# Performance work log

Measured on AMD Instinct MI355X. Metric: run time of the kernel, lower is better.

Reference implementation:

```python
import jax, jax.numpy as jnp
import numpy as np

PAGE_SIZE = 64  # page size of the 64-token page table (get_page_table_64)


def setup_inputs() -> dict:
    key = jax.random.key(0)
    k1, k2, k3, k4 = jax.random.split(key, 4)
    b, h, d = 64, 64, 128
    num_blocks = 128
    num_pages = b * num_blocks
    query = jax.random.normal(k1, (b, h, d), dtype=jnp.float32)
    weights = jax.random.normal(k2, (b, h), dtype=jnp.float32)
    index_k_cache = jax.random.normal(k3, (num_pages, PAGE_SIZE, d), dtype=jnp.float32)
    # each batch row gets its own distinct pages (all indices in range)
    block_tables = jnp.arange(b * num_blocks, dtype=jnp.int32).reshape(b, num_blocks)
    seq_lens = jax.random.randint(k4, (b,), 1, num_blocks * PAGE_SIZE, dtype=jnp.int32)
    return {
        "query": query,
        "weights": weights,
        "index_k_cache": index_k_cache,
        "block_tables": block_tables,
        "seq_lens": seq_lens,
    }


def reference(query, weights, index_k_cache, block_tables, seq_lens):
    # Faithful translation of triton_mqa_logits_kernel (paged MQA ReLU-weighted
    # QK logits for the top-k indexer).
    b, h, d = query.shape
    num_blocks = block_tables.shape[1]
    max_seq_len = num_blocks * PAGE_SIZE
    # Gather paged KV per block table: [b, num_blocks, PAGE, d] -> [b, S, d]
    k = index_k_cache[block_tables].reshape(b, max_seq_len, d)
    # s[b,h,s] = q . k  (MQA: single K shared across index heads)
    s = jnp.einsum("bhd,bsd->bhs", query, k)
    # ReLU then per-head weighted sum over heads -> [b, S]
    logits = jnp.einsum("bh,bhs->bs", weights, jax.nn.relu(s))
    # positions beyond the sequence length are invalid (-inf, as in the ragged
    # path all_qk_logits init, so downstream top-k never selects them)
    pos = jnp.arange(max_seq_len, dtype=jnp.int32)
    mask = pos[None, :] < seq_lens[:, None]
    return jnp.where(mask, logits, -jnp.inf).astype(jnp.float32)
```

## Files before the change

kernel.cpp:

```cpp
#include <hip/hip_runtime.h>
#include <hip/hip_bf16.h>

#define B 64
#define H 64
#define D 128
#define NB 128
#define PAGE 64
#define SMAX (NB * PAGE)
#define TILE_S 64
#define NEG_BIG (-3.0e38f)

typedef __attribute__((ext_vector_type(8))) short bf16x8;
typedef __attribute__((ext_vector_type(4))) float f32x4;

__device__ __forceinline__ unsigned int rnd16(float f) {
    union { float f; unsigned int u; } v; v.f = f;
    return v.u + 0x8000u;
}
__device__ __forceinline__ unsigned int pack2(float lo, float hi) {
    return __builtin_amdgcn_perm(rnd16(hi), rnd16(lo), 0x07060302);
}
__device__ __forceinline__ bf16x8 cvt8(float4 a, float4 b) {
    union { unsigned int u[4]; bf16x8 v; } r;
    r.u[0] = pack2(a.x, a.y); r.u[1] = pack2(a.z, a.w);
    r.u[2] = pack2(b.x, b.y); r.u[3] = pack2(b.z, b.w);
    return r.v;
}

__device__ __forceinline__ void load_lds16(const void* g, void* l) {
    __builtin_amdgcn_global_load_lds(
        (const __attribute__((address_space(1))) unsigned int*)g,
        (__attribute__((address_space(3))) unsigned int*)l,
        16, 0, 0);
}

__global__ __launch_bounds__(256) void q_prep(
    const float* __restrict__ query, unsigned int* __restrict__ qws)
{
    const int b = blockIdx.x >> 2, i = blockIdx.x & 3, tid = threadIdx.x;
    const float* qb = query + (size_t)b * H * D;
    unsigned int* ob = qws + (size_t)b * 4096;
    const int idx = i * 256 + tid;
    const int h = idx >> 4, c = idx & 15;
    const float4 f0 = *(const float4*)(qb + h * D + c * 8);
    const float4 f1 = *(const float4*)(qb + h * D + c * 8 + 4);
    uint4 o;
    o.x = pack2(f0.x, f0.y); o.y = pack2(f0.z, f0.w);
    o.z = pack2(f1.x, f1.y); o.w = pack2(f1.z, f1.w);
    *(uint4*)(ob + (h * 16 + (c ^ (h & 15))) * 4) = o;
}

__global__ __launch_bounds__(256) void indexer_kernel(
    const unsigned int* __restrict__ qws,
    const float* __restrict__ weights,
    const float* __restrict__ kcache,
    const int*   __restrict__ block_tables,
    const int*   __restrict__ seq_lens,
    float*       __restrict__ out)
{
    const int b    = blockIdx.y;
    const int tile = blockIdx.x;
    const int tid  = threadIdx.x;
    const int slen = seq_lens[b];

    if (tile * TILE_S >= slen) {
        if (tid < TILE_S)
            out[(size_t)b * SMAX + tile * TILE_S + tid] = NEG_BIG;
        return;
    }

    __shared__ __align__(16) float k_lds[TILE_S * D];
    __shared__ __align__(16) unsigned short q_lds[H * 16 * 8];

    const int wv = tid >> 6, ln = tid & 63;
    const int quad = ln >> 4, lm = ln & 15;

    const int page = block_tables[b * NB + tile];
    const float* pbase = kcache + (size_t)page * PAGE * D;

    #pragma unroll
    for (int j = 0; j < 8; ++j) {
        const int r  = wv * 16 + j * 2 + (ln >> 5);
        const int cs = ln & 31;
        const int cg = cs ^ (r & 15);
        load_lds16(pbase + r * D + cg * 4, &k_lds[(wv * 16 + j * 2) * D]);
    }
    {
        const unsigned int* src = qws + (size_t)b * 4096 + wv * 1024;
        #pragma unroll
        for (int j = 0; j < 4; ++j)
            load_lds16(src + j * 256 + ln * 4,
                       &q_lds[(wv * 1024 + j * 256) * 2]);
    }
    __syncthreads();

    const int wbase = tile * TILE_S + wv * 16;
    if (wbase >= slen) {
        if (ln < 16) out[(size_t)b * SMAX + wbase + ln] = NEG_BIG;
        return;
    }

    f32x4 acc[4] = {};
    #pragma unroll
    for (int kc = 0; kc < 4; ++kc) {
        const int row = wv * 16 + lm;
        const int c0  = kc * 8 + quad * 2;
        const float4 f0 = *(const float4*)&k_lds[row * D + ((c0    ) ^ lm) * 4];
        const float4 f1 = *(const float4*)&k_lds[row * D + ((c0 + 1) ^ lm) * 4];
        const bf16x8 a = cvt8(f0, f1);
        #pragma unroll
        for (int ni = 0; ni < 4; ++ni) {
            const int slot = (ni * 16 + lm) * 16 + ((kc * 4 + quad) ^ lm);
            const bf16x8 q = *(const bf16x8*)&q_lds[slot * 8];
            acc[ni] = __builtin_amdgcn_mfma_f32_16x16x32_bf16(a, q, acc[ni], 0, 0, 0);
        }
    }

    float w[4];
    #pragma unroll
    for (int ni = 0; ni < 4; ++ni)
        w[ni] = weights[b * H + ni * 16 + lm];

    #pragma unroll
    for (int r = 0; r < 4; ++r) {
        float v = 0.f;
        #pragma unroll
        for (int ni = 0; ni < 4; ++ni)
            v = fmaf(w[ni], fmaxf(acc[ni][r], 0.f), v);
        v += __shfl_xor(v, 1);
        v += __shfl_xor(v, 2);
        v += __shfl_xor(v, 4);
        v += __shfl_xor(v, 8);
        if (lm == 0) {
            const int pos = wbase + quad * 4 + r;
            out[(size_t)b * SMAX + pos] = (pos < slen) ? v : NEG_BIG;
        }
    }
}

extern "C" void kernel_launch(void* const* d_in, const int* in_sizes, int n_in,
                              void* d_out, int out_size, void* d_ws, size_t ws_size,
                              hipStream_t stream) {
    const float* query   = (const float*)d_in[0];
    const float* weights = (const float*)d_in[1];
    const float* kcache  = (const float*)d_in[2];
    const int*   bt      = (const int*)d_in[3];
    const int*   sl      = (const int*)d_in[4];
    float*       out     = (float*)d_out;
    unsigned int* qws    = (unsigned int*)d_ws;

    q_prep<<<B * 4, 256, 0, stream>>>(query, qws);
    dim3 grid(SMAX / TILE_S, B);
    indexer_kernel<<<grid, 256, 0, stream>>>(qws, weights, kcache, bt, sl, out);
}
```

Before: 333.8 us.

## Drop LDS staging; load K and bf16 Q fragments directly from global memory

Removes the shared-memory staging of the K page and Q tile along with the block-wide barrier, so each lane loads its MFMA operands straight from global memory. The Q preprocessing kernel now writes Q in a fragment-ordered layout so that each lane's per-(kc, ni) bf16x8 load is contiguous. This drops the LDS round-trip and sync and lets waves past the sequence end exit before issuing any loads. In exchange, Q fragments are re-read from global/L2 by every block and K loads become per-lane 32-byte strided accesses rather than asynchronous LDS copies.

```diff
diff --git a/kernel.cpp b/kernel.cpp
--- a/kernel.cpp
+++ b/kernel.cpp
@@ -1,5 +1,4 @@
 #include <hip/hip_runtime.h>
-#include <hip/hip_bf16.h>
 
 #define B 64
 #define H 64
@@ -27,27 +26,19 @@
     return r.v;
 }
 
-__device__ __forceinline__ void load_lds16(const void* g, void* l) {
-    __builtin_amdgcn_global_load_lds(
-        (const __attribute__((address_space(1))) unsigned int*)g,
-        (__attribute__((address_space(3))) unsigned int*)l,
-        16, 0, 0);
-}
-
 __global__ __launch_bounds__(256) void q_prep(
     const float* __restrict__ query, unsigned int* __restrict__ qws)
 {
     const int b = blockIdx.x >> 2, i = blockIdx.x & 3, tid = threadIdx.x;
-    const float* qb = query + (size_t)b * H * D;
-    unsigned int* ob = qws + (size_t)b * 4096;
     const int idx = i * 256 + tid;
-    const int h = idx >> 4, c = idx & 15;
-    const float4 f0 = *(const float4*)(qb + h * D + c * 8);
-    const float4 f1 = *(const float4*)(qb + h * D + c * 8 + 4);
+    const int c = idx >> 6, h = idx & 63;
+    const float* src = query + ((size_t)b * H + h) * D + c * 8;
+    const float4 f0 = *(const float4*)(src);
+    const float4 f1 = *(const float4*)(src + 4);
     uint4 o;
     o.x = pack2(f0.x, f0.y); o.y = pack2(f0.z, f0.w);
     o.z = pack2(f1.x, f1.y); o.w = pack2(f1.z, f1.w);
-    *(uint4*)(ob + (h * 16 + (c ^ (h & 15))) * 4) = o;
+    *(uint4*)(qws + ((size_t)b * 1024 + idx) * 4) = o;
 }
 
 __global__ __launch_bounds__(256) void indexer_kernel(
@@ -69,49 +60,29 @@
         return;
     }
 
-    __shared__ __align__(16) float k_lds[TILE_S * D];
-    __shared__ __align__(16) unsigned short q_lds[H * 16 * 8];
-
     const int wv = tid >> 6, ln = tid & 63;
     const int quad = ln >> 4, lm = ln & 15;
-
-    const int page = block_tables[b * NB + tile];
-    const float* pbase = kcache + (size_t)page * PAGE * D;
-
-    #pragma unroll
-    for (int j = 0; j < 8; ++j) {
-        const int r  = wv * 16 + j * 2 + (ln >> 5);
-        const int cs = ln & 31;
-        const int cg = cs ^ (r & 15);
-        load_lds16(pbase + r * D + cg * 4, &k_lds[(wv * 16 + j * 2) * D]);
-    }
-    {
-        const unsigned int* src = qws + (size_t)b * 4096 + wv * 1024;
-        #pragma unroll
-        for (int j = 0; j < 4; ++j)
-            load_lds16(src + j * 256 + ln * 4,
-                       &q_lds[(wv * 1024 + j * 256) * 2]);
-    }
-    __syncthreads();
-
     const int wbase = tile * TILE_S + wv * 16;
     if (wbase >= slen) {
         if (ln < 16) out[(size_t)b * SMAX + wbase + ln] = NEG_BIG;
         return;
     }
 
+    const int page = block_tables[b * NB + tile];
+
+    const float* krow = kcache + (size_t)page * PAGE * D
+                      + (wv * 16 + lm) * D + quad * 8;
+    const unsigned int* qb = qws + (size_t)b * 4096 + quad * 256 + lm * 4;
+
     f32x4 acc[4] = {};
     #pragma unroll
     for (int kc = 0; kc < 4; ++kc) {
-        const int row = wv * 16 + lm;
-        const int c0  = kc * 8 + quad * 2;
-        const float4 f0 = *(const float4*)&k_lds[row * D + ((c0    ) ^ lm) * 4];
-        const float4 f1 = *(const float4*)&k_lds[row * D + ((c0 + 1) ^ lm) * 4];
+        const float4 f0 = *(const float4*)(krow + kc * 32);
+        const float4 f1 = *(const float4*)(krow + kc * 32 + 4);
         const bf16x8 a = cvt8(f0, f1);
         #pragma unroll
         for (int ni = 0; ni < 4; ++ni) {
-            const int slot = (ni * 16 + lm) * 16 + ((kc * 4 + quad) ^ lm);
-            const bf16x8 q = *(const bf16x8*)&q_lds[slot * 8];
+            const bf16x8 q = *(const bf16x8*)(qb + kc * 1024 + ni * 64);
             acc[ni] = __builtin_amdgcn_mfma_f32_16x16x32_bf16(a, q, acc[ni], 0, 0, 0);
         }
     }
```

New measurement: 335.4 us. Within noise of the previous version (+0.5%).
